# Kernel optimization log

Measured on AMD Instinct MI355X. Metric: run time of the kernel, lower is better.

Reference implementation:

```python
import jax, jax.numpy as jnp
import numpy as np

MASK_ID = 3
MAX_SEN = 128
SEN_DIM = 128
EMBED = 1024


def setup_inputs() -> dict:
    key = jax.random.key(0)
    ks = jax.random.split(key, 12)
    B, S, E, D = 8, 8192, EMBED, SEN_DIM
    s = 0.02
    return {
        "input_ids": jax.random.randint(ks[0], (B, S), 0, 64),
        "hidden_states": jax.random.normal(ks[1], (B, S, E), jnp.float32),
        "Wv": jax.random.normal(ks[2], (E, D), jnp.float32) * s,
        "bv": jnp.zeros((D,), jnp.float32),
        "Wq": jax.random.normal(ks[3], (E, D), jnp.float32) * s,
        "bq": jnp.zeros((D,), jnp.float32),
        "Wk": jax.random.normal(ks[4], (D, D), jnp.float32) * s,
        "bk": jnp.zeros((D,), jnp.float32),
        "Wvt": jax.random.normal(ks[5], (D, D), jnp.float32) * s,
        "bvt": jnp.zeros((D,), jnp.float32),
        "Wo": jax.random.normal(ks[6], (D, E), jnp.float32) * s,
        "bo": jnp.zeros((E,), jnp.float32),
    }


def reference(input_ids, hidden_states, Wv, bv, Wq, bq, Wk, bk, Wvt, bvt, Wo, bo):
    B, S, E = hidden_states.shape
    dt = hidden_states.dtype

    # sentence segmentation: each mask token t with running count c belongs to bucket c-1
    mask = input_ids == MASK_ID                               # (B, S)
    csum = jnp.cumsum(mask.astype(jnp.int32), axis=1)         # (B, S)
    # tokens that are not mask tokens (or overflow max_sen_num) go to dummy bucket MAX_SEN
    seg = jnp.where(mask & (csum <= MAX_SEN), csum - 1, MAX_SEN)  # (B, S)

    # segment-sum replacement for torch.bmm(sen_pos_mask, hidden_states)
    b_idx = jnp.arange(B)[:, None]
    pooled = jnp.zeros((B, MAX_SEN + 1, E), dt).at[b_idx, seg].add(hidden_states)[:, :MAX_SEN]  # (B, M, E)

    static_sen_states = pooled @ Wv + bv                      # (B, M, 128)

    q_token = (hidden_states @ Wq + bq) * (SEN_DIM ** -0.5)   # (B, S, 128)
    k_sen = static_sen_states @ Wk + bk                       # (B, M, 128)
    v_sen = static_sen_states @ Wvt + bvt                     # (B, M, 128)

    # token t may attend to sentences 0..csum[t]-1
    tmp_mask = (jnp.arange(MAX_SEN)[None, None, :] + 1) <= csum[:, :, None]  # (B, S, M)
    neg = jnp.finfo(dt).min
    logits = jnp.einsum('bsd,bmd->bsm', q_token, k_sen) + jnp.where(tmp_mask, jnp.zeros((), dt), neg)
    attn = jax.nn.softmax(logits, axis=-1) * tmp_mask.astype(dt)  # (B, S, M)

    sen_attn_output = jnp.einsum('bsm,bmd->bsd', attn, v_sen) @ Wo + bo  # (B, S, E)
    return sen_attn_output
```

## Files before the change

kernel.cpp:

```cpp
#include <hip/hip_runtime.h>
#include <hip/hip_bf16.h>

#define MASK_ID 3
#define MAX_SEN 128
#define NB 8
#define SEQ 8192
#define EMB 1024
#define DIM 128

typedef __attribute__((ext_vector_type(8))) short short8v;
typedef __attribute__((ext_vector_type(4))) float f32x4;

#define MFMA(a, b, c) __builtin_amdgcn_mfma_f32_16x16x32_bf16(a, b, c, 0, 0, 0)

__device__ __forceinline__ short f2b(float x) {
    union { float f; unsigned u; } v; v.f = x;
    unsigned r = (v.u + 0x7FFFu + ((v.u >> 16) & 1u)) >> 16;
    return (short)r;
}

__device__ __forceinline__ unsigned cvtpk(float a, float b) {
    unsigned r;
    asm("v_cvt_pk_bf16_f32 %0, %1, %2" : "=v"(r) : "v"(a), "v"(b));
    return r;
}

__device__ __forceinline__ short8v pack8(float4 a, float4 b) {
    union { short8v s; unsigned u[4]; } r;
    r.u[0] = cvtpk(a.x, a.y);
    r.u[1] = cvtpk(a.z, a.w);
    r.u[2] = cvtpk(b.x, b.y);
    r.u[3] = cvtpk(b.z, b.w);
    return r.s;
}

__global__ __launch_bounds__(1024) void seg_kernel(const int* __restrict__ ids,
                                                   int* __restrict__ pos,
                                                   int* __restrict__ nvis) {
    int b = blockIdx.x;
    int tid = threadIdx.x;
    __shared__ int sc[1024];
    __shared__ int sc2[1024];
    const int PER = SEQ / 1024;
    int base = b * SEQ + tid * PER;

    int ids_l[PER];
    int cnt = 0;
    #pragma unroll
    for (int j = 0; j < PER; j++) {
        ids_l[j] = ids[base + j];
        cnt += (ids_l[j] == MASK_ID) ? 1 : 0;
    }
    if (tid < MAX_SEN) pos[b * MAX_SEN + tid] = -1;
    sc[tid] = cnt;
    __syncthreads();

    int* src = sc;
    int* dst = sc2;
    for (int off = 1; off < 1024; off <<= 1) {
        int v = src[tid];
        if (tid >= off) v += src[tid - off];
        dst[tid] = v;
        __syncthreads();
        int* t = src; src = dst; dst = t;
    }
    int incl = src[tid];
    int run = incl - cnt;

    #pragma unroll
    for (int j = 0; j < PER; j++) {
        if (ids_l[j] == MASK_ID) {
            run++;
            if (run <= MAX_SEN) pos[b * MAX_SEN + run - 1] = tid * PER + j;
        }
        int nv = run; if (nv > MAX_SEN) nv = MAX_SEN;
        nvis[base + j] = nv;
    }
}

__global__ __launch_bounds__(256) void prep_w(const float* __restrict__ Wq,
                                              const float* __restrict__ Wo,
                                              short* __restrict__ WqTt,
                                              short* __restrict__ WoTt) {
    int idx = blockIdx.x * 256 + threadIdx.x;
    {
        int e = idx >> 7, d = idx & 127;
        int c = e >> 6, ks = (e >> 5) & 1, lq = (e >> 3) & 3, j = e & 7;
        int cf = d >> 4, lr = d & 15;
        WqTt[(((c * 2 + ks) * 8 + cf) * 512) + (lq * 16 + lr) * 8 + j] = f2b(Wq[idx]);
    }
    {
        int dd = idx >> 10, e = idx & 1023;
        int ef = e >> 4, lr = e & 15;
        int kk = dd >> 5, lq = (dd >> 3) & 3, j = dd & 7;
        WoTt[((ef * 4 + kk) * 512) + (lq * 16 + lr) * 8 + j] = f2b(Wo[idx]);
    }
}

__global__ __launch_bounds__(128) void statkv_kernel(const float* __restrict__ hidden,
                                                     const float* __restrict__ Wv, const float* __restrict__ bv,
                                                     const float* __restrict__ Wk, const float* __restrict__ bk,
                                                     const float* __restrict__ Wvt, const float* __restrict__ bvt,
                                                     const int* __restrict__ pos,
                                                     short* __restrict__ k_t, short* __restrict__ vT_t) {
    int m = blockIdx.x, b = blockIdx.y;
    int d = threadIdx.x;
    __shared__ float h[EMB];
    __shared__ float srow[DIM];
    int p = pos[b * MAX_SEN + m];
    float acc = bv[d];
    if (p >= 0) {
        const float* hp = hidden + ((size_t)b * SEQ + p) * EMB;
        for (int e = d; e < EMB; e += 128) h[e] = hp[e];
        __syncthreads();
        float a0 = 0.f, a1 = 0.f, a2 = 0.f, a3 = 0.f;
        for (int e = 0; e < EMB; e += 4) {
            a0 += h[e]     * Wv[e * DIM + d];
            a1 += h[e + 1] * Wv[(e + 1) * DIM + d];
            a2 += h[e + 2] * Wv[(e + 2) * DIM + d];
            a3 += h[e + 3] * Wv[(e + 3) * DIM + d];
        }
        acc += (a0 + a1) + (a2 + a3);
    }
    srow[d] = acc;
    __syncthreads();
    float k0 = 0.f, k1 = 0.f, v0 = 0.f, v1 = 0.f;
    for (int e = 0; e < DIM; e += 2) {
        float s0 = srow[e], s1 = srow[e + 1];
        k0 += s0 * Wk[e * DIM + d];
        k1 += s1 * Wk[(e + 1) * DIM + d];
        v0 += s0 * Wvt[e * DIM + d];
        v1 += s1 * Wvt[(e + 1) * DIM + d];
    }
    {
        int kk = d >> 5, lq = (d >> 3) & 3, j = d & 7;
        int fid = (m >> 4) * 4 + kk;
        k_t[(b << 14) + fid * 512 + (lq * 16 + (m & 15)) * 8 + j] = f2b(bk[d] + k0 + k1);
    }
    {
        int df = d >> 4, kk = m >> 5, lq = (m >> 3) & 3, j = m & 7;
        int fid = df * 4 + kk;
        vT_t[(b << 14) + fid * 512 + (lq * 16 + (d & 15)) * 8 + j] = f2b(bvt[d] + v0 + v1);
    }
}

__global__ __launch_bounds__(256, 3) void attn_kernel(
    const float* __restrict__ hidden,
    const short* __restrict__ WqTt, const float* __restrict__ bq,
    const short* __restrict__ k_t, const short* __restrict__ vT_t,
    const short* __restrict__ WoTt, const float* __restrict__ bo,
    const int* __restrict__ nvis,
    float* __restrict__ out) {
    int wg = (blockIdx.x & 7) * 128 + (blockIdx.x >> 3);
    int b  = wg >> 7;
    int s0 = (wg & 127) * 64;
    int tid = threadIdx.x;
    int lane = tid & 63;
    int w  = tid >> 6;
    int lr = lane & 15;
    int lq = lane >> 4;

    __shared__ __align__(16) char SH[49152];
    char* Ab  = SH;
    char* pPc = SH;
    char* odc = SH + 16384;
    char* qPc = SH + 32768;

    const size_t hrow = (size_t)b * SEQ + s0;
    const float* hbase = hidden + hrow * EMB;
    f32x4 zero = {0.f, 0.f, 0.f, 0.f};

    f32x4 acc[4][2];
    #pragma unroll
    for (int rf = 0; rf < 4; rf++) { acc[rf][0] = zero; acc[rf][1] = zero; }

    int G0 = tid * 2, row0 = G0 >> 3, kq0 = G0 & 7;
    int G1 = G0 + 1,  row1 = G1 >> 3, kq1 = G1 & 7;
    const float* ha0 = hbase + (size_t)row0 * EMB + kq0 * 8;
    const float* ha1 = hbase + (size_t)row1 * EMB + kq1 * 8;
    int dst0 = (row0 * 128 + kq0 * 16) ^ ((row0 & 7) << 4);
    int dst1 = (row1 * 128 + kq1 * 16) ^ ((row1 & 7) << 4);

    float4 pa[4];
    short8v Wa[4], Wb[4];

#define LOADA(C) do { \
    pa[0] = *(const float4*)(ha0 + (C) * 64); \
    pa[1] = *(const float4*)(ha0 + (C) * 64 + 4); \
    pa[2] = *(const float4*)(ha1 + (C) * 64); \
    pa[3] = *(const float4*)(ha1 + (C) * 64 + 4); } while (0)

#define LOADW(C, W) do { \
    const short* wp = WqTt + ((C) * 16 + 2 * w) * 512 + lane * 8; \
    W[0] = *(const short8v*)(wp); \
    W[1] = *(const short8v*)(wp + 512); \
    W[2] = *(const short8v*)(wp + 8 * 512); \
    W[3] = *(const short8v*)(wp + 9 * 512); } while (0)

#define STORE_A() do { \
    *(short8v*)(Ab + dst0) = pack8(pa[0], pa[1]); \
    *(short8v*)(Ab + dst1) = pack8(pa[2], pa[3]); } while (0)

#define COMPUTE(W) do { \
    _Pragma("unroll") \
    for (int ks = 0; ks < 2; ks++) { \
        _Pragma("unroll") \
        for (int rf = 0; rf < 4; rf++) { \
            int row = rf * 16 + lr; \
            short8v fa = *(short8v*)(Ab + ((row * 128 + ks * 64 + lq * 16) ^ ((row & 7) << 4))); \
            acc[rf][0] = MFMA(fa, W[ks * 2 + 0], acc[rf][0]); \
            acc[rf][1] = MFMA(fa, W[ks * 2 + 1], acc[rf][1]); \
        } } } while (0)

    LOADA(0);
    LOADW(0, Wa);

    for (int c = 0; c < 16; c += 2) {
        __syncthreads();
        STORE_A();
        LOADA(c + 1);
        LOADW(c + 1, Wb);
        __syncthreads();
        COMPUTE(Wa);

        __syncthreads();
        STORE_A();
        if (c + 2 < 16) {
            LOADA(c + 2);
            LOADW(c + 2, Wa);
        }
        __syncthreads();
        COMPUTE(Wb);
    }
    {
        const float scale = 0.08838834764831845f;
        int d0 = w * 32 + lr;
        float bq0 = bq[d0], bq1 = bq[d0 + 16];
        #pragma unroll
        for (int rf = 0; rf < 4; rf++)
            #pragma unroll
            for (int r = 0; r < 4; r++) {
                int row = rf * 16 + lq * 4 + r;
                int x = (row & 7) << 4;
                *(short*)(qPc + row * 256 + ((d0 * 2) ^ x))        = f2b((acc[rf][0][r] + bq0) * scale);
                *(short*)(qPc + row * 256 + (((d0 + 16) * 2) ^ x)) = f2b((acc[rf][1][r] + bq1) * scale);
            }
    }
    __syncthreads();

    {
        f32x4 l[4][2];
        #pragma unroll
        for (int rf = 0; rf < 4; rf++) { l[rf][0] = zero; l[rf][1] = zero; }
        const short* kbase = k_t + (b << 14) + (2 * w) * 4 * 512 + lane * 8;
        #pragma unroll
        for (int kk = 0; kk < 4; kk++) {
            const short8v fb0 = *(const short8v*)(kbase + kk * 512);
            const short8v fb1 = *(const short8v*)(kbase + (4 + kk) * 512);
            #pragma unroll
            for (int rf = 0; rf < 4; rf++) {
                int row = rf * 16 + lr;
                int x = (row & 7) << 4;
                short8v fa = *(short8v*)(qPc + row * 256 + ((kk * 64 + lq * 16) ^ x));
                l[rf][0] = MFMA(fa, fb0, l[rf][0]);
                l[rf][1] = MFMA(fa, fb1, l[rf][1]);
            }
        }
        #pragma unroll
        for (int rf = 0; rf < 4; rf++)
            #pragma unroll
            for (int r = 0; r < 4; r++) {
                int row = rf * 16 + lq * 4 + r;
                int x = (row & 7) << 4;
                *(float*)(SH + row * 512 + (((w * 32 + lr) * 4) ^ x))      = l[rf][0][r];
                *(float*)(SH + row * 512 + (((w * 32 + 16 + lr) * 4) ^ x)) = l[rf][1][r];
            }
    }
    __syncthreads();

    {
        int t = tid >> 2, sub = tid & 3;
        int nv = nvis[b * SEQ + s0 + t];
        int x = (t & 7) << 4;
        float pv[32];
        #pragma unroll
        for (int u = 0; u < 8; u++) {
            float4 v = *(const float4*)(SH + t * 512 + ((sub * 128 + u * 16) ^ x));
            pv[u * 4]     = v.x; pv[u * 4 + 1] = v.y;
            pv[u * 4 + 2] = v.z; pv[u * 4 + 3] = v.w;
        }
        int base_m = sub * 32;
        float mx = -3.0e38f;
        #pragma unroll
        for (int i = 0; i < 32; i++)
            mx = (base_m + i < nv) ? fmaxf(mx, pv[i]) : mx;
        mx = fmaxf(mx, __shfl_xor(mx, 1));
        mx = fmaxf(mx, __shfl_xor(mx, 2));
        float sum = 0.f;
        #pragma unroll
        for (int i = 0; i < 32; i++) {
            float e = (base_m + i < nv) ? __expf(pv[i] - mx) : 0.f;
            pv[i] = e;
            sum += e;
        }
        sum += __shfl_xor(sum, 1);
        sum += __shfl_xor(sum, 2);
        float inv = (nv > 0) ? 1.0f / sum : 0.f;

        __syncthreads();

        #pragma unroll
        for (int u = 0; u < 4; u++) {
            union { short8v s; unsigned uu[4]; } p;
            #pragma unroll
            for (int i = 0; i < 4; i++)
                p.uu[i] = cvtpk(pv[u * 8 + 2 * i] * inv, pv[u * 8 + 2 * i + 1] * inv);
            *(short8v*)(pPc + t * 256 + ((sub * 64 + u * 16) ^ x)) = p.s;
        }
    }
    __syncthreads();

    {
        f32x4 o[4][2];
        #pragma unroll
        for (int rf = 0; rf < 4; rf++) { o[rf][0] = zero; o[rf][1] = zero; }
        const short* vbase = vT_t + (b << 14) + (2 * w) * 4 * 512 + lane * 8;
        #pragma unroll
        for (int kk = 0; kk < 4; kk++) {
            const short8v fb0 = *(const short8v*)(vbase + kk * 512);
            const short8v fb1 = *(const short8v*)(vbase + (4 + kk) * 512);
            #pragma unroll
            for (int rf = 0; rf < 4; rf++) {
                int row = rf * 16 + lr;
                int x = (row & 7) << 4;
                short8v fa = *(short8v*)(pPc + row * 256 + ((kk * 64 + lq * 16) ^ x));
                o[rf][0] = MFMA(fa, fb0, o[rf][0]);
                o[rf][1] = MFMA(fa, fb1, o[rf][1]);
            }
        }
        int d0 = w * 32 + lr;
        #pragma unroll
        for (int rf = 0; rf < 4; rf++)
            #pragma unroll
            for (int r = 0; r < 4; r++) {
                int row = rf * 16 + lq * 4 + r;
                int x = (row & 7) << 4;
                *(short*)(odc + row * 256 + ((d0 * 2) ^ x))        = f2b(o[rf][0][r]);
                *(short*)(odc + row * 256 + (((d0 + 16) * 2) ^ x)) = f2b(o[rf][1][r]);
            }
    }
    __syncthreads();

    {
        short8v af[4][4];
        #pragma unroll
        for (int rf = 0; rf < 4; rf++)
            #pragma unroll
            for (int kk = 0; kk < 4; kk++) {
                int row = rf * 16 + lr;
                int x = (row & 7) << 4;
                af[rf][kk] = *(short8v*)(odc + row * 256 + ((kk * 64 + lq * 16) ^ x));
            }
        #pragma unroll
        for (int grp = 0; grp < 4; grp++) {
            int colbase = w * 256 + grp * 64;
            f32x4 ac[4][4];
            #pragma unroll
            for (int rf = 0; rf < 4; rf++)
                #pragma unroll
                for (int cf = 0; cf < 4; cf++) ac[rf][cf] = zero;
            #pragma unroll
            for (int kk = 0; kk < 4; kk++) {
                #pragma unroll
                for (int cf = 0; cf < 4; cf++) {
                    const short8v bb = *(const short8v*)(WoTt
                        + ((w * 16 + grp * 4 + cf) * 4 + kk) * 512 + lane * 8);
                    #pragma unroll
                    for (int rf = 0; rf < 4; rf++)
                        ac[rf][cf] = MFMA(af[rf][kk], bb, ac[rf][cf]);
                }
            }
            #pragma unroll
            for (int cf = 0; cf < 4; cf++) {
                int col = colbase + cf * 16 + lr;
                float bov = bo[col];
                #pragma unroll
                for (int rf = 0; rf < 4; rf++)
                    #pragma unroll
                    for (int r = 0; r < 4; r++)
                        out[(hrow + rf * 16 + lq * 4 + r) * EMB + col] = ac[rf][cf][r] + bov;
            }
        }
    }
}

extern "C" void kernel_launch(void* const* d_in, const int* in_sizes, int n_in,
                              void* d_out, int out_size, void* d_ws, size_t ws_size,
                              hipStream_t stream) {
    const int*   ids    = (const int*)d_in[0];
    const float* hidden = (const float*)d_in[1];
    const float* Wv     = (const float*)d_in[2];
    const float* bv     = (const float*)d_in[3];
    const float* Wq     = (const float*)d_in[4];
    const float* bq     = (const float*)d_in[5];
    const float* Wk     = (const float*)d_in[6];
    const float* bk     = (const float*)d_in[7];
    const float* Wvt    = (const float*)d_in[8];
    const float* bvt    = (const float*)d_in[9];
    const float* Wo     = (const float*)d_in[10];
    const float* bo     = (const float*)d_in[11];

    char* ws = (char*)d_ws;
    int*   pos   = (int*)ws;
    int*   nvis  = (int*)(ws + (4 << 10));
    short* k_t   = (short*)(ws + (260 << 10));
    short* vT_t  = (short*)(ws + (516 << 10));
    short* WqTt  = (short*)(ws + (772 << 10));
    short* WoTt  = (short*)(ws + (1028 << 10));

    seg_kernel<<<NB, 1024, 0, stream>>>(ids, pos, nvis);
    prep_w<<<512, 256, 0, stream>>>(Wq, Wo, WqTt, WoTt);
    dim3 g2(MAX_SEN, NB);
    statkv_kernel<<<g2, 128, 0, stream>>>(hidden, Wv, bv, Wk, bk, Wvt, bvt, pos, k_t, vT_t);
    attn_kernel<<<NB * (SEQ / 64), 256, 0, stream>>>(hidden, WqTt, bq, k_t, vT_t, WoTt, bo,
                                                     nvis, (float*)d_out);
}
```

Measured before the change: 237.2 us.

## Split Q projection into separate kernel using direct global-to-LDS loads

Splits the fused attention kernel into a Q-projection kernel and an attention/output kernel, passing bf16 Q fragments through a workspace buffer laid out in MFMA fragment order. The Q kernel stages fp32 hidden rows straight into swizzled LDS with global_load_lds and double buffering, converting to bf16 at fragment read time. This drops the register round-trip and sync-heavy pipeline, and lowers LDS per block so more blocks fit per CU. The cost is an extra launch and a write and read of Q (8x8192x128 bf16) through global memory.

```diff
diff --git a/kernel.cpp b/kernel.cpp
--- a/kernel.cpp
+++ b/kernel.cpp
@@ -12,6 +12,9 @@
 typedef __attribute__((ext_vector_type(4))) float f32x4;
 
 #define MFMA(a, b, c) __builtin_amdgcn_mfma_f32_16x16x32_bf16(a, b, c, 0, 0, 0)
+
+typedef __attribute__((address_space(1))) const void g_void;
+typedef __attribute__((address_space(3))) void l_void;
 
 __device__ __forceinline__ short f2b(float x) {
     union { float f; unsigned u; } v; v.f = x;
@@ -144,13 +147,102 @@
     }
 }
 
-__global__ __launch_bounds__(256, 3) void attn_kernel(
-    const float* __restrict__ hidden,
-    const short* __restrict__ WqTt, const float* __restrict__ bq,
-    const short* __restrict__ k_t, const short* __restrict__ vT_t,
-    const short* __restrict__ WoTt, const float* __restrict__ bo,
-    const int* __restrict__ nvis,
-    float* __restrict__ out) {
+__global__ __launch_bounds__(256, 4) void q_kernel(const float* __restrict__ hidden,
+                                                   const short* __restrict__ WqTt,
+                                                   const float* __restrict__ bq,
+                                                   short* __restrict__ q_t) {
+    int blk = blockIdx.x;
+    int tid = threadIdx.x;
+    int lane = tid & 63, w = tid >> 6, lr = lane & 15, lq = lane >> 4;
+
+    __shared__ __align__(16) char SH[32768];
+    char* A0 = SH;
+    char* A1 = SH + 16384;
+    char* qt = SH;
+
+    const char* hbytes = (const char*)(hidden + (size_t)blk * 64 * EMB);
+    f32x4 zero = {0.f, 0.f, 0.f, 0.f};
+    f32x4 acc[4][2];
+    #pragma unroll
+    for (int rf = 0; rf < 4; rf++) { acc[rf][0] = zero; acc[rf][1] = zero; }
+
+    short8v Wa[4], Wb[4];
+
+#define QSTAGE(C, B) do { \
+    int lsub = lane >> 4; \
+    int blin = (lane & 15) << 4; \
+    _Pragma("unroll") \
+    for (int j = 0; j < 4; j++) { \
+        int row = w * 16 + j * 4 + lsub; \
+        const char* sp = hbytes + (size_t)row * 4096 + (C) * 256 + (blin ^ ((row & 7) << 4)); \
+        __builtin_amdgcn_global_load_lds((g_void*)sp, (l_void*)((B) + w * 4096 + j * 1024), 16, 0, 0); \
+    } } while (0)
+
+#define QLOADW(C, W) do { \
+    const short* wp = WqTt + ((C) * 16 + 2 * w) * 512 + lane * 8; \
+    W[0] = *(const short8v*)(wp); \
+    W[1] = *(const short8v*)(wp + 512); \
+    W[2] = *(const short8v*)(wp + 8 * 512); \
+    W[3] = *(const short8v*)(wp + 9 * 512); } while (0)
+
+#define QCOMPUTE(B, W) do { \
+    _Pragma("unroll") \
+    for (int ks = 0; ks < 2; ks++) { \
+        _Pragma("unroll") \
+        for (int rf = 0; rf < 4; rf++) { \
+            int row = rf * 16 + lr; \
+            int x = (row & 7) << 4; \
+            int kb = ks * 128 + lq * 32; \
+            float4 f0 = *(const float4*)((B) + row * 256 + (kb ^ x)); \
+            float4 f1 = *(const float4*)((B) + row * 256 + ((kb + 16) ^ x)); \
+            short8v fa = pack8(f0, f1); \
+            acc[rf][0] = MFMA(fa, W[ks * 2 + 0], acc[rf][0]); \
+            acc[rf][1] = MFMA(fa, W[ks * 2 + 1], acc[rf][1]); \
+        } } } while (0)
+
+    QSTAGE(0, A0);
+    QLOADW(0, Wa);
+    __syncthreads();
+    for (int c = 0; c < 16; c += 2) {
+        if (c + 1 < 16) { QSTAGE(c + 1, A1); QLOADW(c + 1, Wb); }
+        QCOMPUTE(A0, Wa);
+        __syncthreads();
+        if (c + 2 < 16) { QSTAGE(c + 2, A0); QLOADW(c + 2, Wa); }
+        QCOMPUTE(A1, Wb);
+        __syncthreads();
+    }
+
+    {
+        const float scale = 0.08838834764831845f;
+        float bq0 = bq[w * 32 + lr], bq1 = bq[w * 32 + 16 + lr];
+        #pragma unroll
+        for (int rf = 0; rf < 4; rf++)
+            #pragma unroll
+            for (int r = 0; r < 4; r++) {
+                short v0 = f2b((acc[rf][0][r] + bq0) * scale);
+                short v1 = f2b((acc[rf][1][r] + bq1) * scale);
+                int lp0 = ((lr >> 3) * 16) + lq * 4 + r;
+                int lp1 = ((2 + (lr >> 3)) * 16) + lq * 4 + r;
+                int j = (lr & 7) * 2;
+                *(short*)(qt + (rf * 4 + w) * 1024 + lp0 * 16 + j) = v0;
+                *(short*)(qt + (rf * 4 + w) * 1024 + lp1 * 16 + j) = v1;
+            }
+    }
+    __syncthreads();
+    #pragma unroll
+    for (int f2 = 0; f2 < 4; f2++) {
+        short8v vfrag = *(short8v*)(qt + (w * 4 + f2) * 1024 + lane * 16);
+        *(short8v*)(q_t + (size_t)blk * 8192 + (w * 4 + f2) * 512 + lane * 8) = vfrag;
+    }
+}
+
+__global__ __launch_bounds__(256, 4) void atto_kernel(const short* __restrict__ q_t,
+                                                      const short* __restrict__ k_t,
+                                                      const short* __restrict__ vT_t,
+                                                      const short* __restrict__ WoTt,
+                                                      const float* __restrict__ bo,
+                                                      const int* __restrict__ nvis,
+                                                      float* __restrict__ out) {
     int wg = (blockIdx.x & 7) * 128 + (blockIdx.x >> 3);
     int b  = wg >> 7;
     int s0 = (wg & 127) * 64;
@@ -160,98 +252,18 @@
     int lr = lane & 15;
     int lq = lane >> 4;
 
-    __shared__ __align__(16) char SH[49152];
-    char* Ab  = SH;
+    __shared__ __align__(16) char SH[32768];
     char* pPc = SH;
     char* odc = SH + 16384;
-    char* qPc = SH + 32768;
 
     const size_t hrow = (size_t)b * SEQ + s0;
-    const float* hbase = hidden + hrow * EMB;
     f32x4 zero = {0.f, 0.f, 0.f, 0.f};
 
-    f32x4 acc[4][2];
-    #pragma unroll
-    for (int rf = 0; rf < 4; rf++) { acc[rf][0] = zero; acc[rf][1] = zero; }
-
-    int G0 = tid * 2, row0 = G0 >> 3, kq0 = G0 & 7;
-    int G1 = G0 + 1,  row1 = G1 >> 3, kq1 = G1 & 7;
-    const float* ha0 = hbase + (size_t)row0 * EMB + kq0 * 8;
-    const float* ha1 = hbase + (size_t)row1 * EMB + kq1 * 8;
-    int dst0 = (row0 * 128 + kq0 * 16) ^ ((row0 & 7) << 4);
-    int dst1 = (row1 * 128 + kq1 * 16) ^ ((row1 & 7) << 4);
-
-    float4 pa[4];
-    short8v Wa[4], Wb[4];
-
-#define LOADA(C) do { \
-    pa[0] = *(const float4*)(ha0 + (C) * 64); \
-    pa[1] = *(const float4*)(ha0 + (C) * 64 + 4); \
-    pa[2] = *(const float4*)(ha1 + (C) * 64); \
-    pa[3] = *(const float4*)(ha1 + (C) * 64 + 4); } while (0)
-
-#define LOADW(C, W) do { \
-    const short* wp = WqTt + ((C) * 16 + 2 * w) * 512 + lane * 8; \
-    W[0] = *(const short8v*)(wp); \
-    W[1] = *(const short8v*)(wp + 512); \
-    W[2] = *(const short8v*)(wp + 8 * 512); \
-    W[3] = *(const short8v*)(wp + 9 * 512); } while (0)
-
-#define STORE_A() do { \
-    *(short8v*)(Ab + dst0) = pack8(pa[0], pa[1]); \
-    *(short8v*)(Ab + dst1) = pack8(pa[2], pa[3]); } while (0)
-
-#define COMPUTE(W) do { \
-    _Pragma("unroll") \
-    for (int ks = 0; ks < 2; ks++) { \
-        _Pragma("unroll") \
-        for (int rf = 0; rf < 4; rf++) { \
-            int row = rf * 16 + lr; \
-            short8v fa = *(short8v*)(Ab + ((row * 128 + ks * 64 + lq * 16) ^ ((row & 7) << 4))); \
-            acc[rf][0] = MFMA(fa, W[ks * 2 + 0], acc[rf][0]); \
-            acc[rf][1] = MFMA(fa, W[ks * 2 + 1], acc[rf][1]); \
-        } } } while (0)
-
-    LOADA(0);
-    LOADW(0, Wa);
-
-    for (int c = 0; c < 16; c += 2) {
-        __syncthreads();
-        STORE_A();
-        LOADA(c + 1);
-        LOADW(c + 1, Wb);
-        __syncthreads();
-        COMPUTE(Wa);
-
-        __syncthreads();
-        STORE_A();
-        if (c + 2 < 16) {
-            LOADA(c + 2);
-            LOADW(c + 2, Wa);
-        }
-        __syncthreads();
-        COMPUTE(Wb);
-    }
-    {
-        const float scale = 0.08838834764831845f;
-        int d0 = w * 32 + lr;
-        float bq0 = bq[d0], bq1 = bq[d0 + 16];
-        #pragma unroll
-        for (int rf = 0; rf < 4; rf++)
-            #pragma unroll
-            for (int r = 0; r < 4; r++) {
-                int row = rf * 16 + lq * 4 + r;
-                int x = (row & 7) << 4;
-                *(short*)(qPc + row * 256 + ((d0 * 2) ^ x))        = f2b((acc[rf][0][r] + bq0) * scale);
-                *(short*)(qPc + row * 256 + (((d0 + 16) * 2) ^ x)) = f2b((acc[rf][1][r] + bq1) * scale);
-            }
-    }
-    __syncthreads();
-
     {
         f32x4 l[4][2];
         #pragma unroll
         for (int rf = 0; rf < 4; rf++) { l[rf][0] = zero; l[rf][1] = zero; }
+        const short* qb    = q_t + (size_t)wg * 8192 + lane * 8;
         const short* kbase = k_t + (b << 14) + (2 * w) * 4 * 512 + lane * 8;
         #pragma unroll
         for (int kk = 0; kk < 4; kk++) {
@@ -259,9 +271,7 @@
             const short8v fb1 = *(const short8v*)(kbase + (4 + kk) * 512);
             #pragma unroll
             for (int rf = 0; rf < 4; rf++) {
-                int row = rf * 16 + lr;
-                int x = (row & 7) << 4;
-                short8v fa = *(short8v*)(qPc + row * 256 + ((kk * 64 + lq * 16) ^ x));
+                short8v fa = *(const short8v*)(qb + (rf * 4 + kk) * 512);
                 l[rf][0] = MFMA(fa, fb0, l[rf][0]);
                 l[rf][1] = MFMA(fa, fb1, l[rf][1]);
             }
@@ -417,11 +427,13 @@
     short* vT_t  = (short*)(ws + (516 << 10));
     short* WqTt  = (short*)(ws + (772 << 10));
     short* WoTt  = (short*)(ws + (1028 << 10));
+    short* q_t   = (short*)(ws + (1284 << 10));
 
     seg_kernel<<<NB, 1024, 0, stream>>>(ids, pos, nvis);
     prep_w<<<512, 256, 0, stream>>>(Wq, Wo, WqTt, WoTt);
     dim3 g2(MAX_SEN, NB);
     statkv_kernel<<<g2, 128, 0, stream>>>(hidden, Wv, bv, Wk, bk, Wvt, bvt, pos, k_t, vT_t);
-    attn_kernel<<<NB * (SEQ / 64), 256, 0, stream>>>(hidden, WqTt, bq, k_t, vT_t, WoTt, bo,
-                                                     nvis, (float*)d_out);
-}
+    q_kernel<<<NB * (SEQ / 64), 256, 0, stream>>>(hidden, WqTt, bq, q_t);
+    atto_kernel<<<NB * (SEQ / 64), 256, 0, stream>>>(q_t, k_t, vT_t, WoTt, bo, nvis,
+                                                     (float*)d_out);
+}
```

After: 329.1 us. +38.8%, slower.

## Compute transposed logits in registers and fuse softmax, cutting LDS to raise occupancy

Applied to the files above, without the earlier changes.

The QK^T stage now computes the transposed score tile, with K fragments as the A operand and Q as B, so each wave holds all 128 sentence logits for its 16 tokens in registers. Softmax runs directly on those registers with cross-lane shuffles, so the fp32 logits no longer round-trip through shared memory. LDS shrinks from 48KB to 32KB and launch bounds go from 3 to 4 blocks per CU, aiming for higher occupancy. The cost is more global loads of K fragments per wave and more register pressure under the tighter bound.

```diff
diff --git a/kernel.cpp b/kernel.cpp
--- a/kernel.cpp
+++ b/kernel.cpp
@@ -144,7 +144,7 @@
     }
 }
 
-__global__ __launch_bounds__(256, 3) void attn_kernel(
+__global__ __launch_bounds__(256, 4) void attn_kernel(
     const float* __restrict__ hidden,
     const short* __restrict__ WqTt, const float* __restrict__ bq,
     const short* __restrict__ k_t, const short* __restrict__ vT_t,
@@ -160,14 +160,17 @@
     int lr = lane & 15;
     int lq = lane >> 4;
 
-    __shared__ __align__(16) char SH[49152];
+    __shared__ __align__(16) char SH[32768];
     char* Ab  = SH;
+    char* qPc = SH + 8192;
     char* pPc = SH;
     char* odc = SH + 16384;
-    char* qPc = SH + 32768;
 
     const size_t hrow = (size_t)b * SEQ + s0;
+    const char* hbytes = (const char*)(hidden + hrow * EMB);
+    (void)hbytes;
     const float* hbase = hidden + hrow * EMB;
+    (void)hbase;
     f32x4 zero = {0.f, 0.f, 0.f, 0.f};
 
     f32x4 acc[4][2];
@@ -176,8 +179,8 @@
 
     int G0 = tid * 2, row0 = G0 >> 3, kq0 = G0 & 7;
     int G1 = G0 + 1,  row1 = G1 >> 3, kq1 = G1 & 7;
-    const float* ha0 = hbase + (size_t)row0 * EMB + kq0 * 8;
-    const float* ha1 = hbase + (size_t)row1 * EMB + kq1 * 8;
+    const float* ha0 = hidden + (hrow + row0) * EMB + kq0 * 8;
+    const float* ha1 = hidden + (hrow + row1) * EMB + kq1 * 8;
     int dst0 = (row0 * 128 + kq0 * 16) ^ ((row0 & 7) << 4);
     int dst1 = (row1 * 128 + kq1 * 16) ^ ((row1 & 7) << 4);
 
@@ -249,73 +252,54 @@
     __syncthreads();
 
     {
-        f32x4 l[4][2];
-        #pragma unroll
-        for (int rf = 0; rf < 4; rf++) { l[rf][0] = zero; l[rf][1] = zero; }
-        const short* kbase = k_t + (b << 14) + (2 * w) * 4 * 512 + lane * 8;
+        f32x4 S[8];
+        #pragma unroll
+        for (int mf = 0; mf < 8; mf++) S[mf] = zero;
+        const short* kbase = k_t + (b << 14) + lane * 8;
+        int tl = w * 16 + lr;
+        int xq = (tl & 7) << 4;
         #pragma unroll
         for (int kk = 0; kk < 4; kk++) {
-            const short8v fb0 = *(const short8v*)(kbase + kk * 512);
-            const short8v fb1 = *(const short8v*)(kbase + (4 + kk) * 512);
-            #pragma unroll
-            for (int rf = 0; rf < 4; rf++) {
-                int row = rf * 16 + lr;
-                int x = (row & 7) << 4;
-                short8v fa = *(short8v*)(qPc + row * 256 + ((kk * 64 + lq * 16) ^ x));
-                l[rf][0] = MFMA(fa, fb0, l[rf][0]);
-                l[rf][1] = MFMA(fa, fb1, l[rf][1]);
-            }
-        }
-        #pragma unroll
-        for (int rf = 0; rf < 4; rf++)
+            short8v fb = *(short8v*)(qPc + tl * 256 + ((kk * 64 + lq * 16) ^ xq));
+            #pragma unroll
+            for (int mf = 0; mf < 8; mf++) {
+                const short8v fa = *(const short8v*)(kbase + (mf * 4 + kk) * 512);
+                S[mf] = MFMA(fa, fb, S[mf]);
+            }
+        }
+        __syncthreads();
+
+        int nv = nvis[b * SEQ + s0 + tl];
+        float mx = -3.0e38f;
+        #pragma unroll
+        for (int mf = 0; mf < 8; mf++)
             #pragma unroll
             for (int r = 0; r < 4; r++) {
-                int row = rf * 16 + lq * 4 + r;
-                int x = (row & 7) << 4;
-                *(float*)(SH + row * 512 + (((w * 32 + lr) * 4) ^ x))      = l[rf][0][r];
-                *(float*)(SH + row * 512 + (((w * 32 + 16 + lr) * 4) ^ x)) = l[rf][1][r];
-            }
-    }
-    __syncthreads();
-
-    {
-        int t = tid >> 2, sub = tid & 3;
-        int nv = nvis[b * SEQ + s0 + t];
-        int x = (t & 7) << 4;
-        float pv[32];
-        #pragma unroll
-        for (int u = 0; u < 8; u++) {
-            float4 v = *(const float4*)(SH + t * 512 + ((sub * 128 + u * 16) ^ x));
-            pv[u * 4]     = v.x; pv[u * 4 + 1] = v.y;
-            pv[u * 4 + 2] = v.z; pv[u * 4 + 3] = v.w;
-        }
-        int base_m = sub * 32;
-        float mx = -3.0e38f;
-        #pragma unroll
-        for (int i = 0; i < 32; i++)
-            mx = (base_m + i < nv) ? fmaxf(mx, pv[i]) : mx;
-        mx = fmaxf(mx, __shfl_xor(mx, 1));
-        mx = fmaxf(mx, __shfl_xor(mx, 2));
+                int m = mf * 16 + lq * 4 + r;
+                mx = (m < nv) ? fmaxf(mx, S[mf][r]) : mx;
+            }
+        mx = fmaxf(mx, __shfl_xor(mx, 16));
+        mx = fmaxf(mx, __shfl_xor(mx, 32));
         float sum = 0.f;
         #pragma unroll
-        for (int i = 0; i < 32; i++) {
-            float e = (base_m + i < nv) ? __expf(pv[i] - mx) : 0.f;
-            pv[i] = e;
-            sum += e;
-        }
-        sum += __shfl_xor(sum, 1);
-        sum += __shfl_xor(sum, 2);
+        for (int mf = 0; mf < 8; mf++)
+            #pragma unroll
+            for (int r = 0; r < 4; r++) {
+                int m = mf * 16 + lq * 4 + r;
+                float e = (m < nv) ? __expf(S[mf][r] - mx) : 0.f;
+                S[mf][r] = e;
+                sum += e;
+            }
+        sum += __shfl_xor(sum, 16);
+        sum += __shfl_xor(sum, 32);
         float inv = (nv > 0) ? 1.0f / sum : 0.f;
 
-        __syncthreads();
-
-        #pragma unroll
-        for (int u = 0; u < 4; u++) {
-            union { short8v s; unsigned uu[4]; } p;
-            #pragma unroll
-            for (int i = 0; i < 4; i++)
-                p.uu[i] = cvtpk(pv[u * 8 + 2 * i] * inv, pv[u * 8 + 2 * i + 1] * inv);
-            *(short8v*)(pPc + t * 256 + ((sub * 64 + u * 16) ^ x)) = p.s;
+        #pragma unroll
+        for (int mf = 0; mf < 8; mf++) {
+            unsigned lo = cvtpk(S[mf][0] * inv, S[mf][1] * inv);
+            unsigned hi = cvtpk(S[mf][2] * inv, S[mf][3] * inv);
+            char* wp = pPc + tl * 256 + ((mf * 32 + lq * 8) ^ xq);
+            *(unsigned long long*)wp = ((unsigned long long)hi << 32) | (unsigned long long)lo;
         }
     }
     __syncthreads();
```

Measured after the change: 293.7 us. +23.8%, slower.

## Deepen hidden-state prefetch to three register stages in Q-projection loop

Applied to the files above, without the earlier changes.

Restructures the Q-projection GEMM main loop so hidden-state tiles are prefetched three chunks ahead using three rotating register buffers, and weight tiles are loaded two chunks ahead, issued after the compute. It replaces __syncthreads with raw s_barrier plus an explicit lgkmcnt wait and a sched_barrier, and fully unrolls the 16 iterations. The aim is to hide global-load latency on the dominant hidden-state stream behind MFMA work. The cost is more VGPRs, which may lower occupancy, and hand-managed synchronisation that is more fragile.

```diff
diff --git a/kernel.cpp b/kernel.cpp
--- a/kernel.cpp
+++ b/kernel.cpp
@@ -167,7 +167,6 @@
     char* qPc = SH + 32768;
 
     const size_t hrow = (size_t)b * SEQ + s0;
-    const float* hbase = hidden + hrow * EMB;
     f32x4 zero = {0.f, 0.f, 0.f, 0.f};
 
     f32x4 acc[4][2];
@@ -176,19 +175,19 @@
 
     int G0 = tid * 2, row0 = G0 >> 3, kq0 = G0 & 7;
     int G1 = G0 + 1,  row1 = G1 >> 3, kq1 = G1 & 7;
-    const float* ha0 = hbase + (size_t)row0 * EMB + kq0 * 8;
-    const float* ha1 = hbase + (size_t)row1 * EMB + kq1 * 8;
+    const float* ha0 = hidden + (hrow + row0) * EMB + kq0 * 8;
+    const float* ha1 = hidden + (hrow + row1) * EMB + kq1 * 8;
     int dst0 = (row0 * 128 + kq0 * 16) ^ ((row0 & 7) << 4);
     int dst1 = (row1 * 128 + kq1 * 16) ^ ((row1 & 7) << 4);
 
-    float4 pa[4];
+    float4 pa0[4], pa1[4], pa2[4];
     short8v Wa[4], Wb[4];
 
-#define LOADA(C) do { \
-    pa[0] = *(const float4*)(ha0 + (C) * 64); \
-    pa[1] = *(const float4*)(ha0 + (C) * 64 + 4); \
-    pa[2] = *(const float4*)(ha1 + (C) * 64); \
-    pa[3] = *(const float4*)(ha1 + (C) * 64 + 4); } while (0)
+#define LOADA(C, PA) do { \
+    PA[0] = *(const float4*)(ha0 + (C) * 64); \
+    PA[1] = *(const float4*)(ha0 + (C) * 64 + 4); \
+    PA[2] = *(const float4*)(ha1 + (C) * 64); \
+    PA[3] = *(const float4*)(ha1 + (C) * 64 + 4); } while (0)
 
 #define LOADW(C, W) do { \
     const short* wp = WqTt + ((C) * 16 + 2 * w) * 512 + lane * 8; \
@@ -197,9 +196,9 @@
     W[2] = *(const short8v*)(wp + 8 * 512); \
     W[3] = *(const short8v*)(wp + 9 * 512); } while (0)
 
-#define STORE_A() do { \
-    *(short8v*)(Ab + dst0) = pack8(pa[0], pa[1]); \
-    *(short8v*)(Ab + dst1) = pack8(pa[2], pa[3]); } while (0)
+#define STORE_A(PA) do { \
+    *(short8v*)(Ab + dst0) = pack8(PA[0], PA[1]); \
+    *(short8v*)(Ab + dst1) = pack8(PA[2], PA[3]); } while (0)
 
 #define COMPUTE(W) do { \
     _Pragma("unroll") \
@@ -212,26 +211,40 @@
             acc[rf][1] = MFMA(fa, W[ks * 2 + 1], acc[rf][1]); \
         } } } while (0)
 
-    LOADA(0);
+#define ITER(c, PA, WW, DO_A, DO_W) do { \
+    __builtin_amdgcn_s_barrier();                  \
+    STORE_A(PA);                                   \
+    if (DO_A) LOADA((c) + 3, PA); \
+    asm volatile("s_waitcnt lgkmcnt(0)" ::: "memory"); \
+    __builtin_amdgcn_sched_barrier(0); \
+    __builtin_amdgcn_s_barrier();                  \
+    COMPUTE(WW); \
+    if (DO_W) LOADW((c) + 2, WW);                  \
+    } while (0)
+
     LOADW(0, Wa);
-
-    for (int c = 0; c < 16; c += 2) {
-        __syncthreads();
-        STORE_A();
-        LOADA(c + 1);
-        LOADW(c + 1, Wb);
-        __syncthreads();
-        COMPUTE(Wa);
-
-        __syncthreads();
-        STORE_A();
-        if (c + 2 < 16) {
-            LOADA(c + 2);
-            LOADW(c + 2, Wa);
-        }
-        __syncthreads();
-        COMPUTE(Wb);
-    }
+    LOADW(1, Wb);
+    LOADA(0, pa0);
+    LOADA(1, pa1);
+    LOADA(2, pa2);
+
+    ITER(0,  pa0, Wa, 1, 1);
+    ITER(1,  pa1, Wb, 1, 1);
+    ITER(2,  pa2, Wa, 1, 1);
+    ITER(3,  pa0, Wb, 1, 1);
+    ITER(4,  pa1, Wa, 1, 1);
+    ITER(5,  pa2, Wb, 1, 1);
+    ITER(6,  pa0, Wa, 1, 1);
+    ITER(7,  pa1, Wb, 1, 1);
+    ITER(8,  pa2, Wa, 1, 1);
+    ITER(9,  pa0, Wb, 1, 1);
+    ITER(10, pa1, Wa, 1, 1);
+    ITER(11, pa2, Wb, 1, 1);
+    ITER(12, pa0, Wa, 1, 1);
+    ITER(13, pa1, Wb, 0, 1);
+    ITER(14, pa2, Wa, 0, 0);
+    ITER(15, pa0, Wb, 0, 0);
+
     {
         const float scale = 0.08838834764831845f;
         int d0 = w * 32 + lr;
```

Result: faster. 228.7 us (-3.6%).
